# Kernel tuning notes

Hardware: AMD Instinct MI355X
Metric: run time of the kernel (lower is better)

The kernel has to match this reference:

```python
import jax, jax.numpy as jnp
import numpy as np

K, C, W, PAD, B = 64, 64, 128, 4, 16  # faces processed, channels, face width, pad, batch
W2 = W + 2 * PAD


def setup_inputs() -> dict:
    key = jax.random.key(0)
    k1, k2, k3, k4, k5, k6 = jax.random.split(key, 6)
    cube = jax.random.normal(k1, (K, C, W, W), dtype=jnp.float32)
    # to_process: sorted unique subset of faces from the 6*B face pool
    to_process = jnp.sort(jax.random.permutation(k2, 6 * B)[:K]).astype(jnp.int32)
    pixel_idx_tb = jax.random.randint(k3, (6, C, 2 * PAD, W2), 0, C * W * W, dtype=jnp.int32)
    pixel_idx_lr = jax.random.randint(k4, (6, C, W, 2 * PAD), 0, C * W * W, dtype=jnp.int32)
    face_idx_tb = jax.random.randint(k5, (6, 2 * PAD, W2), 0, 6, dtype=jnp.int32)
    face_idx_lr = jax.random.randint(k6, (6, W, 2 * PAD), 0, 6, dtype=jnp.int32)
    return {
        "cube": cube,
        "to_process": to_process,
        "batch_size": B,
        "pixel_idx_tb": pixel_idx_tb,
        "pixel_idx_lr": pixel_idx_lr,
        "face_idx_tb": face_idx_tb,
        "face_idx_lr": face_idx_lr,
    }


def reference(cube, to_process, batch_size, pixel_idx_tb, pixel_idx_lr, face_idx_tb, face_idx_lr):
    k, c, w, _ = cube.shape
    p = PAD
    # inverse map: global face id -> row in cube, -1 if not processed
    inv = jnp.full((6 * batch_size,), -1, dtype=jnp.int32).at[to_process].set(
        jnp.arange(k, dtype=jnp.int32))
    flat_cube = cube.reshape(-1)  # (k*c*w*w,)

    def pad_block(face_idx, pixel_idx):
        # face_idx: (6, *sp), pixel_idx: (6, c, *sp)
        f = face_idx[None] + 6 * jnp.arange(batch_size, dtype=jnp.int32).reshape(-1, 1, 1, 1)
        f = f.reshape((6 * batch_size,) + face_idx.shape[1:])[to_process]  # (k, *sp)
        f = inv[f]  # -1 where neighbor face not processed
        px = pixel_idx[to_process % 6]  # (k, c, *sp)
        idx = f[:, None] * (c * w * w) + px  # (k, c, *sp)
        mask = idx >= 0
        g = jnp.take(flat_cube, jnp.maximum(idx, 0), axis=0)
        return jnp.where(mask, g, jnp.zeros((), cube.dtype))

    pad_tb = pad_block(face_idx_tb, pixel_idx_tb)  # (k, c, 2p, w+2p)
    pad_lr = pad_block(face_idx_lr, pixel_idx_lr)  # (k, c, w, 2p)

    padded = jnp.concatenate([pad_lr[:, :, :, :p], cube, pad_lr[:, :, :, p:]], axis=3)
    padded = jnp.concatenate([pad_tb[:, :, :p, :], padded, pad_tb[:, :, p:, :]], axis=2)
    return padded  # (k, c, w+2p, w+2p)
```

## Files before the change

### kernel.cpp

```cpp
#include <hip/hip_runtime.h>

#define K_   64
#define C_   64
#define W_   128
#define P_   4
#define B_   16
#define W2_  136
#define OUTSP 18496
#define CWW  1048576

#define N_INT 16777216
#define N_TB  1114112
#define N_HALO_UNITS 33792
#define N_UNITS (N_HALO_UNITS * 9)
#define N_WID   (N_UNITS * 64)

typedef int   int4n   __attribute__((ext_vector_type(4)));
typedef float float4n __attribute__((ext_vector_type(4)));

__global__ void fused_pad_kernel(const float* __restrict__ cube,
                                 const int* __restrict__ to_process,
                                 const int* __restrict__ px_tb,
                                 const int* __restrict__ px_lr,
                                 const int* __restrict__ fi_tb,
                                 const int* __restrict__ fi_lr,
                                 float* __restrict__ out) {
    __shared__ int inv[6 * B_];
    __shared__ int tp[K_];
    const int tid = threadIdx.x;
    if (tid < 6 * B_) inv[tid] = -1;
    if (tid < K_)     tp[tid]  = to_process[tid];
    __syncthreads();
    if (tid < K_)     inv[tp[tid]] = tid;
    __syncthreads();

    const int stride = gridDim.x * blockDim.x;
    for (int t = blockIdx.x * blockDim.x + tid; t < N_WID; t += stride) {
        int U = t >> 6;
        int l = t & 63;
        int g = U / 9;
        int r = U - 9 * g;

        if (r < 8) {
            int id = ((g << 3) + r) * 64 + l;
            if (id < N_INT) {
                int q  = id & 31;
                int R  = id >> 5;
                int rr = R & (W_ - 1);
                int kc = R >> 7;
                float4n v = reinterpret_cast<const float4n*>(cube)[id];
                float4n* dst = reinterpret_cast<float4n*>(
                    out + (size_t)kc * OUTSP + (size_t)(rr + P_) * W2_ + P_) + q;
                __builtin_nontemporal_store(v, dst);
            }
        } else {
            int id = (g << 6) + l;
            if (id < N_TB) {
                int col4 = id % 34;
                int rest = id / 34;
                int rr   = rest & 7;  rest >>= 3;
                int cc   = rest & 63;
                int kk   = rest >> 6;

                int gf = tp[kk];
                int b  = gf / 6;
                int fb = gf - 6 * b;
                int4n fiv = *reinterpret_cast<const int4n*>(
                    fi_tb + (fb * 2 * P_ + rr) * W2_ + col4 * 4);
                int4n pxv = *reinterpret_cast<const int4n*>(
                    px_tb + (((fb * C_ + cc) * 2 * P_) + rr) * W2_ + col4 * 4);

                float4n v;
                int f0 = inv[fiv.x + 6 * b];
                int f1 = inv[fiv.y + 6 * b];
                int f2 = inv[fiv.z + 6 * b];
                int f3 = inv[fiv.w + 6 * b];
                v.x = (f0 >= 0) ? cube[(size_t)f0 * CWW + pxv.x] : 0.0f;
                v.y = (f1 >= 0) ? cube[(size_t)f1 * CWW + pxv.y] : 0.0f;
                v.z = (f2 >= 0) ? cube[(size_t)f2 * CWW + pxv.z] : 0.0f;
                v.w = (f3 >= 0) ? cube[(size_t)f3 * CWW + pxv.w] : 0.0f;

                int outr = (rr < P_) ? rr : (W_ + rr);
                float4n* dst = reinterpret_cast<float4n*>(
                    out + (size_t)(kk * C_ + cc) * OUTSP + (size_t)outr * W2_ + col4 * 4);
                __builtin_nontemporal_store(v, dst);
            } else {
                int u  = id - N_TB;
                int q  = u & 1;
                int rr = (u >> 1) & (W_ - 1);
                int cc = (u >> 8) & 63;
                int kk = u >> 14;

                int gf = tp[kk];
                int b  = gf / 6;
                int fb = gf - 6 * b;
                int4n fiv = *reinterpret_cast<const int4n*>(
                    fi_lr + (fb * W_ + rr) * 2 * P_ + q * 4);
                int4n pxv = *reinterpret_cast<const int4n*>(
                    px_lr + ((fb * C_ + cc) * W_ + rr) * 2 * P_ + q * 4);

                float4n v;
                int f0 = inv[fiv.x + 6 * b];
                int f1 = inv[fiv.y + 6 * b];
                int f2 = inv[fiv.z + 6 * b];
                int f3 = inv[fiv.w + 6 * b];
                v.x = (f0 >= 0) ? cube[(size_t)f0 * CWW + pxv.x] : 0.0f;
                v.y = (f1 >= 0) ? cube[(size_t)f1 * CWW + pxv.y] : 0.0f;
                v.z = (f2 >= 0) ? cube[(size_t)f2 * CWW + pxv.z] : 0.0f;
                v.w = (f3 >= 0) ? cube[(size_t)f3 * CWW + pxv.w] : 0.0f;

                int outc = q ? (W_ + P_) : 0;
                float4n* dst = reinterpret_cast<float4n*>(
                    out + (size_t)(kk * C_ + cc) * OUTSP + (size_t)(rr + P_) * W2_ + outc);
                __builtin_nontemporal_store(v, dst);
            }
        }
    }
}

extern "C" void kernel_launch(void* const* d_in, const int* in_sizes, int n_in,
                              void* d_out, int out_size, void* d_ws, size_t ws_size,
                              hipStream_t stream) {
    const float* cube         = (const float*)d_in[0];
    const int*   to_process   = (const int*)d_in[1];
    const int*   pixel_idx_tb = (const int*)d_in[3];
    const int*   pixel_idx_lr = (const int*)d_in[4];
    const int*   face_idx_tb  = (const int*)d_in[5];
    const int*   face_idx_lr  = (const int*)d_in[6];
    float*       out          = (float*)d_out;

    fused_pad_kernel<<<2048, 256, 0, stream>>>(
        cube, to_process, pixel_idx_tb, pixel_idx_lr,
        face_idx_tb, face_idx_lr, out);
}
```

Before: 217.0 us.

## Split pad kernel into two phases by source-face half for cache locality

Splits the fused copy-and-gather kernel into two launches. Each launch copies half of the cube interior and gathers only the halo elements whose source face lies in that half, with unprocessed-face zeros written in phase 0. The aim is to keep each phase's random gathers within a working set small enough to stay resident in cache. In exchange, every phase re-reads all halo indices, the vector halo stores become scalar, and an extra kernel launch is added.

```diff
diff --git a/kernel.cpp b/kernel.cpp
--- a/kernel.cpp
+++ b/kernel.cpp
@@ -9,22 +9,24 @@
 #define OUTSP 18496
 #define CWW  1048576
 
-#define N_INT 16777216
-#define N_TB  1114112
-#define N_HALO_UNITS 33792
-#define N_UNITS (N_HALO_UNITS * 9)
-#define N_WID   (N_UNITS * 64)
+#define NQ_TB     1114112
+#define NQ_HALO   2162688
+#define NU_INT_PH 131072
+#define NU_HALO_U 33792
+#define N_UNITS_PH (NU_HALO_U * 5)
+#define N_WID_PH   (N_UNITS_PH * 64)
 
 typedef int   int4n   __attribute__((ext_vector_type(4)));
 typedef float float4n __attribute__((ext_vector_type(4)));
 
-__global__ void fused_pad_kernel(const float* __restrict__ cube,
-                                 const int* __restrict__ to_process,
-                                 const int* __restrict__ px_tb,
-                                 const int* __restrict__ px_lr,
-                                 const int* __restrict__ fi_tb,
-                                 const int* __restrict__ fi_lr,
-                                 float* __restrict__ out) {
+__global__ void fused_pad_phase_kernel(const float* __restrict__ cube,
+                                       const int* __restrict__ to_process,
+                                       const int* __restrict__ px_tb,
+                                       const int* __restrict__ px_lr,
+                                       const int* __restrict__ fi_tb,
+                                       const int* __restrict__ fi_lr,
+                                       float* __restrict__ out,
+                                       int phase) {
     __shared__ int inv[6 * B_];
     __shared__ int tp[K_];
     const int tid = threadIdx.x;
@@ -35,15 +37,16 @@
     __syncthreads();
 
     const int stride = gridDim.x * blockDim.x;
-    for (int t = blockIdx.x * blockDim.x + tid; t < N_WID; t += stride) {
+    for (int t = blockIdx.x * blockDim.x + tid; t < N_WID_PH; t += stride) {
         int U = t >> 6;
         int l = t & 63;
-        int g = U / 9;
-        int r = U - 9 * g;
+        int g = U / 5;
+        int r = U - 5 * g;
 
-        if (r < 8) {
-            int id = ((g << 3) + r) * 64 + l;
-            if (id < N_INT) {
+        if (r < 4) {
+            int iu = (g << 2) + r;
+            if (iu < NU_INT_PH) {
+                int id = (phase << 23) + (iu << 6) + l;
                 int q  = id & 31;
                 int R  = id >> 5;
                 int rr = R & (W_ - 1);
@@ -54,65 +57,62 @@
                 __builtin_nontemporal_store(v, dst);
             }
         } else {
-            int id = (g << 6) + l;
-            if (id < N_TB) {
-                int col4 = id % 34;
-                int rest = id / 34;
-                int rr   = rest & 7;  rest >>= 3;
-                int cc   = rest & 63;
-                int kk   = rest >> 6;
+            int hq = (g << 6) + l;
+            if (hq < NQ_TB) {
+                int col4 = hq % 34;
+                int rest = hq / 34;
+                int rr   = rest & 7;
+                int cc   = (rest >> 3) & 63;
+                int kk   = rest >> 9;
 
                 int gf = tp[kk];
-                int b  = gf / 6;
-                int fb = gf - 6 * b;
+                int b6 = 6 * (gf / 6);
+                int fb = gf - b6;
                 int4n fiv = *reinterpret_cast<const int4n*>(
                     fi_tb + (fb * 2 * P_ + rr) * W2_ + col4 * 4);
                 int4n pxv = *reinterpret_cast<const int4n*>(
-                    px_tb + (((fb * C_ + cc) * 2 * P_) + rr) * W2_ + col4 * 4);
-
-                float4n v;
-                int f0 = inv[fiv.x + 6 * b];
-                int f1 = inv[fiv.y + 6 * b];
-                int f2 = inv[fiv.z + 6 * b];
-                int f3 = inv[fiv.w + 6 * b];
-                v.x = (f0 >= 0) ? cube[(size_t)f0 * CWW + pxv.x] : 0.0f;
-                v.y = (f1 >= 0) ? cube[(size_t)f1 * CWW + pxv.y] : 0.0f;
-                v.z = (f2 >= 0) ? cube[(size_t)f2 * CWW + pxv.z] : 0.0f;
-                v.w = (f3 >= 0) ? cube[(size_t)f3 * CWW + pxv.w] : 0.0f;
+                    px_tb + ((fb * C_ + cc) * 2 * P_ + rr) * W2_ + col4 * 4);
 
                 int outr = (rr < P_) ? rr : (W_ + rr);
-                float4n* dst = reinterpret_cast<float4n*>(
-                    out + (size_t)(kk * C_ + cc) * OUTSP + (size_t)outr * W2_ + col4 * 4);
-                __builtin_nontemporal_store(v, dst);
+                float* obase = out + (size_t)(kk * C_ + cc) * OUTSP
+                                   + (size_t)outr * W2_ + col4 * 4;
+#pragma unroll
+                for (int e = 0; e < 4; ++e) {
+                    int fe = inv[((const int*)&fiv)[e] + b6];
+                    bool own = (fe < 0) ? (phase == 0) : ((fe >> 5) == phase);
+                    if (own) {
+                        float v = (fe >= 0)
+                            ? cube[(size_t)fe * CWW + ((const int*)&pxv)[e]] : 0.0f;
+                        __builtin_nontemporal_store(v, obase + e);
+                    }
+                }
             } else {
-                int u  = id - N_TB;
+                int u  = hq - NQ_TB;
                 int q  = u & 1;
                 int rr = (u >> 1) & (W_ - 1);
                 int cc = (u >> 8) & 63;
                 int kk = u >> 14;
 
                 int gf = tp[kk];
-                int b  = gf / 6;
-                int fb = gf - 6 * b;
+                int b6 = 6 * (gf / 6);
+                int fb = gf - b6;
                 int4n fiv = *reinterpret_cast<const int4n*>(
                     fi_lr + (fb * W_ + rr) * 2 * P_ + q * 4);
                 int4n pxv = *reinterpret_cast<const int4n*>(
                     px_lr + ((fb * C_ + cc) * W_ + rr) * 2 * P_ + q * 4);
 
-                float4n v;
-                int f0 = inv[fiv.x + 6 * b];
-                int f1 = inv[fiv.y + 6 * b];
-                int f2 = inv[fiv.z + 6 * b];
-                int f3 = inv[fiv.w + 6 * b];
-                v.x = (f0 >= 0) ? cube[(size_t)f0 * CWW + pxv.x] : 0.0f;
-                v.y = (f1 >= 0) ? cube[(size_t)f1 * CWW + pxv.y] : 0.0f;
-                v.z = (f2 >= 0) ? cube[(size_t)f2 * CWW + pxv.z] : 0.0f;
-                v.w = (f3 >= 0) ? cube[(size_t)f3 * CWW + pxv.w] : 0.0f;
-
-                int outc = q ? (W_ + P_) : 0;
-                float4n* dst = reinterpret_cast<float4n*>(
-                    out + (size_t)(kk * C_ + cc) * OUTSP + (size_t)(rr + P_) * W2_ + outc);
-                __builtin_nontemporal_store(v, dst);
+                float* obase = out + (size_t)(kk * C_ + cc) * OUTSP
+                                   + (size_t)(rr + P_) * W2_ + (q ? (W_ + P_) : 0);
+#pragma unroll
+                for (int e = 0; e < 4; ++e) {
+                    int fe = inv[((const int*)&fiv)[e] + b6];
+                    bool own = (fe < 0) ? (phase == 0) : ((fe >> 5) == phase);
+                    if (own) {
+                        float v = (fe >= 0)
+                            ? cube[(size_t)fe * CWW + ((const int*)&pxv)[e]] : 0.0f;
+                        __builtin_nontemporal_store(v, obase + e);
+                    }
+                }
             }
         }
     }
@@ -129,7 +129,10 @@
     const int*   face_idx_lr  = (const int*)d_in[6];
     float*       out          = (float*)d_out;
 
-    fused_pad_kernel<<<2048, 256, 0, stream>>>(
+    fused_pad_phase_kernel<<<2048, 256, 0, stream>>>(
         cube, to_process, pixel_idx_tb, pixel_idx_lr,
-        face_idx_tb, face_idx_lr, out);
+        face_idx_tb, face_idx_lr, out, 0);
+    fused_pad_phase_kernel<<<2048, 256, 0, stream>>>(
+        cube, to_process, pixel_idx_tb, pixel_idx_lr,
+        face_idx_tb, face_idx_lr, out, 1);
 }
```

New measurement: 319.8 us. 47.4% more time.

## Interleave halo and interior work per face with proportional wave distribution

Applied to the files above, without the earlier changes.

Replaces the fixed 8-interior-to-1-halo wave interleaving with a per-face schedule. Each face gets 4096 interior units and 528 halo units, spread evenly using a 33/289 ratio. Halo indices are reordered so a wave covers one side (top/bottom or left/right) across rows, and left/right units now map 64 lanes to consecutive rows rather than alternating sides. The aim is to keep gather and streaming-copy work balanced and local to a face for better cache and DRAM behavior, at the cost of an extra integer division per iteration.

```diff
diff --git a/kernel.cpp b/kernel.cpp
--- a/kernel.cpp
+++ b/kernel.cpp
@@ -9,11 +9,12 @@
 #define OUTSP 18496
 #define CWW  1048576
 
-#define N_INT 16777216
-#define N_TB  1114112
-#define N_HALO_UNITS 33792
-#define N_UNITS (N_HALO_UNITS * 9)
-#define N_WID   (N_UNITS * 64)
+#define TB_U_PER_K 272
+#define HU_PER_K   528
+#define IU_PER_K   4096
+#define U_PER_K    4624
+#define N_UNITS    (64 * U_PER_K)
+#define N_WID      (N_UNITS * 64)
 
 typedef int   int4n   __attribute__((ext_vector_type(4)));
 typedef float float4n __attribute__((ext_vector_type(4)));
@@ -38,82 +39,83 @@
     for (int t = blockIdx.x * blockDim.x + tid; t < N_WID; t += stride) {
         int U = t >> 6;
         int l = t & 63;
-        int g = U / 9;
-        int r = U - 9 * g;
+        int f = U / U_PER_K;
+        int u = U - f * U_PER_K;
+        int hu  = (u * 33) / 289;
+        bool is_halo = ((u + 1) * 33) / 289 > hu;
 
-        if (r < 8) {
-            int id = ((g << 3) + r) * 64 + l;
-            if (id < N_INT) {
-                int q  = id & 31;
-                int R  = id >> 5;
-                int rr = R & (W_ - 1);
-                int kc = R >> 7;
-                float4n v = reinterpret_cast<const float4n*>(cube)[id];
-                float4n* dst = reinterpret_cast<float4n*>(
-                    out + (size_t)kc * OUTSP + (size_t)(rr + P_) * W2_ + P_) + q;
-                __builtin_nontemporal_store(v, dst);
-            }
+        if (!is_halo) {
+            int iu = u - hu;
+            int id = ((f * IU_PER_K + iu) << 6) + l;
+            int q  = id & 31;
+            int R  = id >> 5;
+            int rr = R & (W_ - 1);
+            int kc = R >> 7;
+            float4n v = reinterpret_cast<const float4n*>(cube)[id];
+            float4n* dst = reinterpret_cast<float4n*>(
+                out + (size_t)kc * OUTSP + (size_t)(rr + P_) * W2_ + P_) + q;
+            __builtin_nontemporal_store(v, dst);
+        } else if (hu < TB_U_PER_K) {
+            int qid  = (f * TB_U_PER_K + hu) * 64 + l;
+            int col4 = qid % 34;
+            int tq   = qid / 34;
+            int rr2  = tq & 3;
+            int cc   = (tq >> 2) & 63;
+            int side = (tq >> 8) & 1;
+            int kk   = tq >> 9;
+            int rr   = side * 4 + rr2;
+
+            int gf = tp[kk];
+            int b6 = 6 * (gf / 6);
+            int fb = gf - b6;
+            int4n fiv = *reinterpret_cast<const int4n*>(
+                fi_tb + (fb * 8 + rr) * W2_ + col4 * 4);
+            int4n pxv = *reinterpret_cast<const int4n*>(
+                px_tb + ((fb * C_ + cc) * 8 + rr) * W2_ + col4 * 4);
+
+            float4n v;
+            int f0 = inv[fiv.x + b6];
+            int f1 = inv[fiv.y + b6];
+            int f2 = inv[fiv.z + b6];
+            int f3 = inv[fiv.w + b6];
+            v.x = (f0 >= 0) ? cube[(size_t)f0 * CWW + pxv.x] : 0.0f;
+            v.y = (f1 >= 0) ? cube[(size_t)f1 * CWW + pxv.y] : 0.0f;
+            v.z = (f2 >= 0) ? cube[(size_t)f2 * CWW + pxv.z] : 0.0f;
+            v.w = (f3 >= 0) ? cube[(size_t)f3 * CWW + pxv.w] : 0.0f;
+
+            int outr = side ? (W_ + P_ + rr2) : rr2;
+            float4n* dst = reinterpret_cast<float4n*>(
+                out + (size_t)(kk * C_ + cc) * OUTSP + (size_t)outr * W2_ + col4 * 4);
+            __builtin_nontemporal_store(v, dst);
         } else {
-            int id = (g << 6) + l;
-            if (id < N_TB) {
-                int col4 = id % 34;
-                int rest = id / 34;
-                int rr   = rest & 7;  rest >>= 3;
-                int cc   = rest & 63;
-                int kk   = rest >> 6;
+            int qid  = (f * 256 + (hu - TB_U_PER_K)) * 64 + l;
+            int r    = qid & 127;
+            int cc   = (qid >> 7) & 63;
+            int side = (qid >> 13) & 1;
+            int kk   = qid >> 14;
 
-                int gf = tp[kk];
-                int b  = gf / 6;
-                int fb = gf - 6 * b;
-                int4n fiv = *reinterpret_cast<const int4n*>(
-                    fi_tb + (fb * 2 * P_ + rr) * W2_ + col4 * 4);
-                int4n pxv = *reinterpret_cast<const int4n*>(
-                    px_tb + (((fb * C_ + cc) * 2 * P_) + rr) * W2_ + col4 * 4);
+            int gf = tp[kk];
+            int b6 = 6 * (gf / 6);
+            int fb = gf - b6;
+            int4n fiv = *reinterpret_cast<const int4n*>(
+                fi_lr + (fb * W_ + r) * 2 * P_ + side * 4);
+            int4n pxv = *reinterpret_cast<const int4n*>(
+                px_lr + ((fb * C_ + cc) * W_ + r) * 2 * P_ + side * 4);
 
-                float4n v;
-                int f0 = inv[fiv.x + 6 * b];
-                int f1 = inv[fiv.y + 6 * b];
-                int f2 = inv[fiv.z + 6 * b];
-                int f3 = inv[fiv.w + 6 * b];
-                v.x = (f0 >= 0) ? cube[(size_t)f0 * CWW + pxv.x] : 0.0f;
-                v.y = (f1 >= 0) ? cube[(size_t)f1 * CWW + pxv.y] : 0.0f;
-                v.z = (f2 >= 0) ? cube[(size_t)f2 * CWW + pxv.z] : 0.0f;
-                v.w = (f3 >= 0) ? cube[(size_t)f3 * CWW + pxv.w] : 0.0f;
+            float4n v;
+            int f0 = inv[fiv.x + b6];
+            int f1 = inv[fiv.y + b6];
+            int f2 = inv[fiv.z + b6];
+            int f3 = inv[fiv.w + b6];
+            v.x = (f0 >= 0) ? cube[(size_t)f0 * CWW + pxv.x] : 0.0f;
+            v.y = (f1 >= 0) ? cube[(size_t)f1 * CWW + pxv.y] : 0.0f;
+            v.z = (f2 >= 0) ? cube[(size_t)f2 * CWW + pxv.z] : 0.0f;
+            v.w = (f3 >= 0) ? cube[(size_t)f3 * CWW + pxv.w] : 0.0f;
 
-                int outr = (rr < P_) ? rr : (W_ + rr);
-                float4n* dst = reinterpret_cast<float4n*>(
-                    out + (size_t)(kk * C_ + cc) * OUTSP + (size_t)outr * W2_ + col4 * 4);
-                __builtin_nontemporal_store(v, dst);
-            } else {
-                int u  = id - N_TB;
-                int q  = u & 1;
-                int rr = (u >> 1) & (W_ - 1);
-                int cc = (u >> 8) & 63;
-                int kk = u >> 14;
-
-                int gf = tp[kk];
-                int b  = gf / 6;
-                int fb = gf - 6 * b;
-                int4n fiv = *reinterpret_cast<const int4n*>(
-                    fi_lr + (fb * W_ + rr) * 2 * P_ + q * 4);
-                int4n pxv = *reinterpret_cast<const int4n*>(
-                    px_lr + ((fb * C_ + cc) * W_ + rr) * 2 * P_ + q * 4);
-
-                float4n v;
-                int f0 = inv[fiv.x + 6 * b];
-                int f1 = inv[fiv.y + 6 * b];
-                int f2 = inv[fiv.z + 6 * b];
-                int f3 = inv[fiv.w + 6 * b];
-                v.x = (f0 >= 0) ? cube[(size_t)f0 * CWW + pxv.x] : 0.0f;
-                v.y = (f1 >= 0) ? cube[(size_t)f1 * CWW + pxv.y] : 0.0f;
-                v.z = (f2 >= 0) ? cube[(size_t)f2 * CWW + pxv.z] : 0.0f;
-                v.w = (f3 >= 0) ? cube[(size_t)f3 * CWW + pxv.w] : 0.0f;
-
-                int outc = q ? (W_ + P_) : 0;
-                float4n* dst = reinterpret_cast<float4n*>(
-                    out + (size_t)(kk * C_ + cc) * OUTSP + (size_t)(rr + P_) * W2_ + outc);
-                __builtin_nontemporal_store(v, dst);
-            }
+            int outc = side ? (W_ + P_) : 0;
+            float4n* dst = reinterpret_cast<float4n*>(
+                out + (size_t)(kk * C_ + cc) * OUTSP + (size_t)(r + P_) * W2_ + outc);
+            __builtin_nontemporal_store(v, dst);
         }
     }
 }
```

Result: no change. 220.1 us (+1.4%).
